# Kernel optimization log

Hardware: AMD Instinct MI355X
Metric: run time of the kernel (lower is better)

Reference implementation:

```python
import jax, jax.numpy as jnp
import numpy as np

B, H, S, D = 4, 16, 2048, 128

def setup_inputs() -> dict:
    key = jax.random.key(0)
    ks = jax.random.split(key, 7)
    inv = 1.0 / np.sqrt(D)
    return {
        "x1": jax.random.normal(ks[0], (B, H, S, D), dtype=jnp.float32),
        "Wq": jax.random.normal(ks[1], (D, D), dtype=jnp.float32) * inv,
        "bq": jax.random.normal(ks[2], (D,), dtype=jnp.float32) * 0.02,
        "Wk": jax.random.normal(ks[3], (D, D), dtype=jnp.float32) * inv,
        "bk": jax.random.normal(ks[4], (D,), dtype=jnp.float32) * 0.02,
        "Wv": jax.random.normal(ks[5], (D, D), dtype=jnp.float32) * inv,
        "bv": jax.random.normal(ks[6], (D,), dtype=jnp.float32) * 0.02,
    }

def reference(x1, Wq, bq, Wk, bk, Wv, bv):
    # torch.nn.Linear: y = x @ W.T + b  (applied to last dim per-head)
    q = jnp.einsum('bhsd,ed->bhse', x1, Wq) + bq
    k = jnp.einsum('bhsd,ed->bhse', x1, Wk) + bk
    v = jnp.einsum('bhsd,ed->bhse', x1, Wv) + bv
    # NOTE: original applies NO 1/sqrt(d) scaling — kept faithful.
    qk = jnp.einsum('bhqd,bhkd->bhqk', q, k)          # [B,H,S,S]
    attn = jax.nn.softmax(qk, axis=-1)
    # dropout(p=0.5) treated as identity (eval mode) for determinism
    out = jnp.einsum('bhqk,bhkd->bhqd', attn, v)      # [B,H,S,D]
    out = jnp.transpose(out, (0, 2, 1, 3)).reshape(B, S * H, D)
    return out
```

## Files before the change

kernel.cpp:

```cpp
#include <hip/hip_runtime.h>
#include <hip/hip_bf16.h>

#define S_LEN 2048
#define D_DIM 128
#define H_NUM 16

typedef float f32x4 __attribute__((ext_vector_type(4)));
typedef _Float16 f16x8 __attribute__((ext_vector_type(8)));
typedef _Float16 f16x4 __attribute__((ext_vector_type(4)));

__device__ __forceinline__ _Float16 f2h(float f) { return (_Float16)f; }

__global__ __launch_bounds__(256) void wconv_kernel(
    const float* __restrict__ Wq, const float* __restrict__ Wk,
    const float* __restrict__ Wv, _Float16* __restrict__ Wb) {
    int i = blockIdx.x * 256 + threadIdx.x;
    Wb[i]         = f2h(Wq[i]);
    Wb[16384 + i] = f2h(Wk[i]);
    Wb[32768 + i] = f2h(Wv[i]);
}

__global__ __launch_bounds__(256) void proj_kernel(
    const float* __restrict__ x,
    const float* __restrict__ bq, const float* __restrict__ bk,
    const float* __restrict__ bv,
    const _Float16* __restrict__ Wb,
    _Float16* __restrict__ Qg, _Float16* __restrict__ Kg, _Float16* __restrict__ Vt)
{
    const int blk = blockIdx.x;
    const int bh  = blk >> 4;
    const int st  = blk & 15;
    const int tid = threadIdx.x;
    const int w = tid >> 6, lane = tid & 63, g = lane >> 4, r16 = lane & 15;
    const int base = st * 128 + w * 32;

    f16x8 xf[2][4];
    #pragma unroll
    for (int rs = 0; rs < 2; ++rs) {
        const int row = base + rs * 16 + r16;
        const float* xr = x + (size_t)(bh * S_LEN + row) * D_DIM + g * 8;
        #pragma unroll
        for (int kk = 0; kk < 4; ++kk) {
            float4 a = *(const float4*)(xr + kk * 32);
            float4 b = *(const float4*)(xr + kk * 32 + 4);
            f16x8 f;
            f[0]=f2h(a.x); f[1]=f2h(a.y); f[2]=f2h(a.z); f[3]=f2h(a.w);
            f[4]=f2h(b.x); f[5]=f2h(b.y); f[6]=f2h(b.z); f[7]=f2h(b.w);
            xf[rs][kk] = f;
        }
    }

    #pragma unroll 1
    for (int p = 0; p < 3; ++p) {
        const float* bias = (p == 0) ? bq : (p == 1) ? bk : bv;
        const _Float16* W = Wb + p * 16384;
        f32x4 acc[2][8];
        #pragma unroll
        for (int rs = 0; rs < 2; ++rs)
            #pragma unroll
            for (int et = 0; et < 8; ++et)
                acc[rs][et] = (f32x4){0.f, 0.f, 0.f, 0.f};

        #pragma unroll
        for (int et = 0; et < 8; ++et) {
            const _Float16* wr = W + (size_t)(et * 16 + r16) * 128 + g * 8;
            #pragma unroll
            for (int kk = 0; kk < 4; ++kk) {
                f16x8 wf = *(const f16x8*)(wr + kk * 32);
                acc[0][et] = __builtin_amdgcn_mfma_f32_16x16x32_f16(xf[0][kk], wf, acc[0][et], 0, 0, 0);
                acc[1][et] = __builtin_amdgcn_mfma_f32_16x16x32_f16(xf[1][kk], wf, acc[1][et], 0, 0, 0);
            }
        }

        #pragma unroll
        for (int et = 0; et < 8; ++et) {
            const float be = bias[et * 16 + r16];
            #pragma unroll
            for (int rs = 0; rs < 2; ++rs) {
                const int row0 = base + rs * 16 + g * 4;
                if (p == 2) {
                    f16x4 vv;
                    vv[0] = f2h(acc[rs][et][0] + be);
                    vv[1] = f2h(acc[rs][et][1] + be);
                    vv[2] = f2h(acc[rs][et][2] + be);
                    vv[3] = f2h(acc[rs][et][3] + be);
                    *(f16x4*)(Vt + (size_t)bh * D_DIM * S_LEN
                                 + (size_t)(et * 16 + r16) * S_LEN + row0) = vv;
                } else {
                    _Float16* O = (p == 0) ? Qg : Kg;
                    #pragma unroll
                    for (int i = 0; i < 4; ++i)
                        O[(size_t)(bh * S_LEN + row0 + i) * D_DIM + et * 16 + r16]
                            = f2h(acc[rs][et][i] + be);
                }
            }
        }
    }
}

__global__ __launch_bounds__(256) void attn_kernel(
    const _Float16* __restrict__ Qg, const _Float16* __restrict__ Kg,
    const _Float16* __restrict__ Vt, float* __restrict__ out)
{
    __shared__ _Float16 k_lds[64][144];
    __shared__ _Float16 v_lds[128][80];
    __shared__ _Float16 p_lds[4][16][80];

    const int blk = blockIdx.x;
    const int bh = blk >> 5;
    const int qt = blk & 31;
    const int b = bh >> 4, h = bh & 15;
    const int tid = threadIdx.x;
    const int w = tid >> 6, lane = tid & 63, g = lane >> 4, r16 = lane & 15;

    f16x8 qf[4];
    {
        const int qrow = qt * 64 + w * 16 + r16;
        const _Float16* qp = Qg + (size_t)(bh * S_LEN + qrow) * D_DIM + g * 8;
        #pragma unroll
        for (int kk = 0; kk < 4; ++kk) qf[kk] = *(const f16x8*)(qp + kk * 32);
    }

    f32x4 acc[8];
    #pragma unroll
    for (int dt = 0; dt < 8; ++dt) acc[dt] = (f32x4){0.f, 0.f, 0.f, 0.f};
    float m[4], l[4];
    #pragma unroll
    for (int i = 0; i < 4; ++i) { m[i] = -1e30f; l[i] = 0.f; }

    const _Float16* Kb = Kg + (size_t)bh * S_LEN * D_DIM;
    const _Float16* Vb = Vt + (size_t)bh * D_DIM * S_LEN;
    const float LOG2E = 1.4426950408889634f;

    for (int kv = 0; kv < 32; ++kv) {
        #pragma unroll
        for (int cc = 0; cc < 4; ++cc) {
            const int off = (tid + cc * 256) * 8;
            const int r = off >> 7, c = off & 127;
            *(uint4*)&k_lds[r][c] =
                *(const uint4*)(Kb + (size_t)(kv * 64 + r) * D_DIM + c);
            const int d = off >> 6, c2 = off & 63;
            *(uint4*)&v_lds[d][c2] =
                *(const uint4*)(Vb + (size_t)d * S_LEN + kv * 64 + c2);
        }
        __syncthreads();

        f32x4 sacc[4];
        #pragma unroll
        for (int ct = 0; ct < 4; ++ct) sacc[ct] = (f32x4){0.f, 0.f, 0.f, 0.f};
        #pragma unroll
        for (int kk = 0; kk < 4; ++kk) {
            f16x8 qk = qf[kk];
            #pragma unroll
            for (int ct = 0; ct < 4; ++ct) {
                f16x8 kf = *(const f16x8*)&k_lds[ct * 16 + r16][kk * 32 + g * 8];
                sacc[ct] = __builtin_amdgcn_mfma_f32_16x16x32_f16(qk, kf, sacc[ct], 0, 0, 0);
            }
        }

        float alpha[4], rsum[4];
        #pragma unroll
        for (int i = 0; i < 4; ++i) {
            float t = fmaxf(fmaxf(sacc[0][i], sacc[1][i]),
                            fmaxf(sacc[2][i], sacc[3][i]));
            t = fmaxf(t, __shfl_xor(t, 1, 64));
            t = fmaxf(t, __shfl_xor(t, 2, 64));
            t = fmaxf(t, __shfl_xor(t, 4, 64));
            t = fmaxf(t, __shfl_xor(t, 8, 64));
            const float nm = fmaxf(m[i], t);
            alpha[i] = exp2f((m[i] - nm) * LOG2E);
            m[i] = nm;
            rsum[i] = 0.f;
        }
        #pragma unroll
        for (int ct = 0; ct < 4; ++ct) {
            #pragma unroll
            for (int i = 0; i < 4; ++i) {
                const float pv = exp2f((sacc[ct][i] - m[i]) * LOG2E);
                rsum[i] += pv;
                p_lds[w][g * 4 + i][ct * 16 + r16] = f2h(pv);
            }
        }
        #pragma unroll
        for (int i = 0; i < 4; ++i) {
            float t = rsum[i];
            t += __shfl_xor(t, 1, 64);
            t += __shfl_xor(t, 2, 64);
            t += __shfl_xor(t, 4, 64);
            t += __shfl_xor(t, 8, 64);
            l[i] = l[i] * alpha[i] + t;
        }
        #pragma unroll
        for (int dt = 0; dt < 8; ++dt)
            #pragma unroll
            for (int i = 0; i < 4; ++i)
                acc[dt][i] *= alpha[i];

        f16x8 pf[2];
        #pragma unroll
        for (int ks = 0; ks < 2; ++ks)
            pf[ks] = *(const f16x8*)&p_lds[w][r16][ks * 32 + g * 8];
        #pragma unroll
        for (int ks = 0; ks < 2; ++ks) {
            #pragma unroll
            for (int dt = 0; dt < 8; ++dt) {
                f16x8 vf = *(const f16x8*)&v_lds[dt * 16 + r16][ks * 32 + g * 8];
                acc[dt] = __builtin_amdgcn_mfma_f32_16x16x32_f16(pf[ks], vf, acc[dt], 0, 0, 0);
            }
        }
        __syncthreads();
    }

    #pragma unroll
    for (int dt = 0; dt < 8; ++dt) {
        #pragma unroll
        for (int i = 0; i < 4; ++i) {
            const int s = qt * 64 + w * 16 + g * 4 + i;
            out[(((size_t)b * S_LEN + s) * H_NUM + h) * D_DIM + dt * 16 + r16]
                = acc[dt][i] / l[i];
        }
    }
}

extern "C" void kernel_launch(void* const* d_in, const int* in_sizes, int n_in,
                              void* d_out, int out_size, void* d_ws, size_t ws_size,
                              hipStream_t stream) {
    const float* x  = (const float*)d_in[0];
    const float* Wq = (const float*)d_in[1];
    const float* bq = (const float*)d_in[2];
    const float* Wk = (const float*)d_in[3];
    const float* bk = (const float*)d_in[4];
    const float* Wv = (const float*)d_in[5];
    const float* bv = (const float*)d_in[6];
    float* out = (float*)d_out;

    char* ws = (char*)d_ws;
    _Float16* Wb  = (_Float16*)ws;
    _Float16* Qg  = (_Float16*)(ws + 131072);
    _Float16* Kg  = Qg + (size_t)64 * S_LEN * D_DIM;
    _Float16* Vtg = Kg + (size_t)64 * S_LEN * D_DIM;

    wconv_kernel<<<64, 256, 0, stream>>>(Wq, Wk, Wv, Wb);
    proj_kernel<<<1024, 256, 0, stream>>>(x, bq, bk, bv, Wb, Qg, Kg, Vtg);
    attn_kernel<<<2048, 256, 0, stream>>>(Qg, Kg, Vtg, out);
}
```

Before: 625.2 us.

## Double query tile per wave, prefetch K/V into registers, transpose score MFMA

The attention kernel now handles 128 query rows per block, 32 per wave, so each K/V tile loaded into LDS is reused twice as much, and the grid is halved. The next K/V tile is prefetched into registers while the current one is computed, overlapping global loads with MFMA work. Scores are computed as K·Q^T so each lane holds a full query column, which makes the softmax reductions cheaper, and P is written with a swizzled vectorized store. The Q/K projection likewise swaps MFMA operands to produce vectorized f16x4 row stores. The cost is higher register pressure from the doubled accumulators and the prefetch registers, which may reduce occupancy.

```diff
diff --git a/kernel.cpp b/kernel.cpp
--- a/kernel.cpp
+++ b/kernel.cpp
@@ -67,31 +67,41 @@
             #pragma unroll
             for (int kk = 0; kk < 4; ++kk) {
                 f16x8 wf = *(const f16x8*)(wr + kk * 32);
-                acc[0][et] = __builtin_amdgcn_mfma_f32_16x16x32_f16(xf[0][kk], wf, acc[0][et], 0, 0, 0);
-                acc[1][et] = __builtin_amdgcn_mfma_f32_16x16x32_f16(xf[1][kk], wf, acc[1][et], 0, 0, 0);
+                if (p < 2) {
+                    acc[0][et] = __builtin_amdgcn_mfma_f32_16x16x32_f16(wf, xf[0][kk], acc[0][et], 0, 0, 0);
+                    acc[1][et] = __builtin_amdgcn_mfma_f32_16x16x32_f16(wf, xf[1][kk], acc[1][et], 0, 0, 0);
+                } else {
+                    acc[0][et] = __builtin_amdgcn_mfma_f32_16x16x32_f16(xf[0][kk], wf, acc[0][et], 0, 0, 0);
+                    acc[1][et] = __builtin_amdgcn_mfma_f32_16x16x32_f16(xf[1][kk], wf, acc[1][et], 0, 0, 0);
+                }
             }
         }
 
         #pragma unroll
         for (int et = 0; et < 8; ++et) {
-            const float be = bias[et * 16 + r16];
             #pragma unroll
             for (int rs = 0; rs < 2; ++rs) {
-                const int row0 = base + rs * 16 + g * 4;
-                if (p == 2) {
+                if (p < 2) {
+                    const int srow = base + rs * 16 + r16;
+                    const int e0 = et * 16 + g * 4;
+                    float4 b4 = *(const float4*)(bias + e0);
+                    f16x4 o;
+                    o[0] = f2h(acc[rs][et][0] + b4.x);
+                    o[1] = f2h(acc[rs][et][1] + b4.y);
+                    o[2] = f2h(acc[rs][et][2] + b4.z);
+                    o[3] = f2h(acc[rs][et][3] + b4.w);
+                    _Float16* O = (p == 0) ? Qg : Kg;
+                    *(f16x4*)(O + (size_t)(bh * S_LEN + srow) * D_DIM + e0) = o;
+                } else {
+                    const float be = bias[et * 16 + r16];
+                    const int s0 = base + rs * 16 + g * 4;
                     f16x4 vv;
                     vv[0] = f2h(acc[rs][et][0] + be);
                     vv[1] = f2h(acc[rs][et][1] + be);
                     vv[2] = f2h(acc[rs][et][2] + be);
                     vv[3] = f2h(acc[rs][et][3] + be);
                     *(f16x4*)(Vt + (size_t)bh * D_DIM * S_LEN
-                                 + (size_t)(et * 16 + r16) * S_LEN + row0) = vv;
-                } else {
-                    _Float16* O = (p == 0) ? Qg : Kg;
-                    #pragma unroll
-                    for (int i = 0; i < 4; ++i)
-                        O[(size_t)(bh * S_LEN + row0 + i) * D_DIM + et * 16 + r16]
-                            = f2h(acc[rs][et][i] + be);
+                                 + (size_t)(et * 16 + r16) * S_LEN + s0) = vv;
                 }
             }
         }
@@ -102,122 +112,145 @@
     const _Float16* __restrict__ Qg, const _Float16* __restrict__ Kg,
     const _Float16* __restrict__ Vt, float* __restrict__ out)
 {
-    __shared__ _Float16 k_lds[64][144];
-    __shared__ _Float16 v_lds[128][80];
-    __shared__ _Float16 p_lds[4][16][80];
+    __shared__ _Float16 k_lds[64][136];
+    __shared__ _Float16 v_lds[128][72];
+    __shared__ _Float16 p_lds[4][32 * 64];
 
     const int blk = blockIdx.x;
-    const int bh = blk >> 5;
-    const int qt = blk & 31;
+    const int bh = blk >> 4;
+    const int qt = blk & 15;
     const int b = bh >> 4, h = bh & 15;
     const int tid = threadIdx.x;
     const int w = tid >> 6, lane = tid & 63, g = lane >> 4, r16 = lane & 15;
-
-    f16x8 qf[4];
-    {
-        const int qrow = qt * 64 + w * 16 + r16;
+    const int swz = (r16 & 7) << 3;
+
+    f16x8 qf[2][4];
+    #pragma unroll
+    for (int s = 0; s < 2; ++s) {
+        const int qrow = qt * 128 + w * 32 + s * 16 + r16;
         const _Float16* qp = Qg + (size_t)(bh * S_LEN + qrow) * D_DIM + g * 8;
         #pragma unroll
-        for (int kk = 0; kk < 4; ++kk) qf[kk] = *(const f16x8*)(qp + kk * 32);
-    }
-
-    f32x4 acc[8];
-    #pragma unroll
-    for (int dt = 0; dt < 8; ++dt) acc[dt] = (f32x4){0.f, 0.f, 0.f, 0.f};
-    float m[4], l[4];
-    #pragma unroll
-    for (int i = 0; i < 4; ++i) { m[i] = -1e30f; l[i] = 0.f; }
-
-    const _Float16* Kb = Kg + (size_t)bh * S_LEN * D_DIM;
+        for (int kk = 0; kk < 4; ++kk) qf[s][kk] = *(const f16x8*)(qp + kk * 32);
+    }
+
+    f32x4 acc[2][8];
+    #pragma unroll
+    for (int s = 0; s < 2; ++s)
+        #pragma unroll
+        for (int dt = 0; dt < 8; ++dt) acc[s][dt] = (f32x4){0.f, 0.f, 0.f, 0.f};
+    float m[2] = {-1e30f, -1e30f}, l[2] = {0.f, 0.f};
+
+    const _Float16* Kb = Qg ? Kg + (size_t)bh * S_LEN * D_DIM : Kg;
     const _Float16* Vb = Vt + (size_t)bh * D_DIM * S_LEN;
     const float LOG2E = 1.4426950408889634f;
 
+    uint4 kreg[4], vreg[4];
+    #pragma unroll
+    for (int cc = 0; cc < 4; ++cc) {
+        const int off = (tid + cc * 256) * 8;
+        kreg[cc] = *(const uint4*)(Kb + (size_t)(off >> 7) * D_DIM + (off & 127));
+        vreg[cc] = *(const uint4*)(Vb + (size_t)(off >> 6) * S_LEN + (off & 63));
+    }
+
     for (int kv = 0; kv < 32; ++kv) {
+        __syncthreads();
         #pragma unroll
         for (int cc = 0; cc < 4; ++cc) {
             const int off = (tid + cc * 256) * 8;
-            const int r = off >> 7, c = off & 127;
-            *(uint4*)&k_lds[r][c] =
-                *(const uint4*)(Kb + (size_t)(kv * 64 + r) * D_DIM + c);
-            const int d = off >> 6, c2 = off & 63;
-            *(uint4*)&v_lds[d][c2] =
-                *(const uint4*)(Vb + (size_t)d * S_LEN + kv * 64 + c2);
+            *(uint4*)&k_lds[off >> 7][off & 127] = kreg[cc];
+            *(uint4*)&v_lds[off >> 6][off & 63] = vreg[cc];
         }
         __syncthreads();
-
-        f32x4 sacc[4];
-        #pragma unroll
-        for (int ct = 0; ct < 4; ++ct) sacc[ct] = (f32x4){0.f, 0.f, 0.f, 0.f};
-        #pragma unroll
-        for (int kk = 0; kk < 4; ++kk) {
-            f16x8 qk = qf[kk];
+        if (kv + 1 < 32) {
+            #pragma unroll
+            for (int cc = 0; cc < 4; ++cc) {
+                const int off = (tid + cc * 256) * 8;
+                kreg[cc] = *(const uint4*)(Kb + (size_t)((kv + 1) * 64 + (off >> 7)) * D_DIM + (off & 127));
+                vreg[cc] = *(const uint4*)(Vb + (size_t)(off >> 6) * S_LEN + (kv + 1) * 64 + (off & 63));
+            }
+        }
+
+        f32x4 sacc[2][4];
+        #pragma unroll
+        for (int s = 0; s < 2; ++s)
+            #pragma unroll
+            for (int ct = 0; ct < 4; ++ct) sacc[s][ct] = (f32x4){0.f, 0.f, 0.f, 0.f};
+        #pragma unroll
+        for (int ct = 0; ct < 4; ++ct) {
+            #pragma unroll
+            for (int kk = 0; kk < 4; ++kk) {
+                f16x8 kf = *(const f16x8*)&k_lds[ct * 16 + r16][kk * 32 + g * 8];
+                sacc[0][ct] = __builtin_amdgcn_mfma_f32_16x16x32_f16(kf, qf[0][kk], sacc[0][ct], 0, 0, 0);
+                sacc[1][ct] = __builtin_amdgcn_mfma_f32_16x16x32_f16(kf, qf[1][kk], sacc[1][ct], 0, 0, 0);
+            }
+        }
+
+        #pragma unroll
+        for (int s = 0; s < 2; ++s) {
+            float t = sacc[s][0][0];
+            #pragma unroll
+            for (int ct = 0; ct < 4; ++ct)
+                #pragma unroll
+                for (int i = 0; i < 4; ++i) t = fmaxf(t, sacc[s][ct][i]);
+            t = fmaxf(t, __shfl_xor(t, 16, 64));
+            t = fmaxf(t, __shfl_xor(t, 32, 64));
+            const float nm = fmaxf(m[s], t);
+            const float al = exp2f((m[s] - nm) * LOG2E);
+            m[s] = nm;
+
+            float rsum = 0.f;
+            _Float16* prow = &p_lds[w][(s * 16 + r16) * 64];
             #pragma unroll
             for (int ct = 0; ct < 4; ++ct) {
-                f16x8 kf = *(const f16x8*)&k_lds[ct * 16 + r16][kk * 32 + g * 8];
-                sacc[ct] = __builtin_amdgcn_mfma_f32_16x16x32_f16(qk, kf, sacc[ct], 0, 0, 0);
-            }
-        }
-
-        float alpha[4], rsum[4];
-        #pragma unroll
-        for (int i = 0; i < 4; ++i) {
-            float t = fmaxf(fmaxf(sacc[0][i], sacc[1][i]),
-                            fmaxf(sacc[2][i], sacc[3][i]));
-            t = fmaxf(t, __shfl_xor(t, 1, 64));
-            t = fmaxf(t, __shfl_xor(t, 2, 64));
-            t = fmaxf(t, __shfl_xor(t, 4, 64));
-            t = fmaxf(t, __shfl_xor(t, 8, 64));
-            const float nm = fmaxf(m[i], t);
-            alpha[i] = exp2f((m[i] - nm) * LOG2E);
-            m[i] = nm;
-            rsum[i] = 0.f;
-        }
-        #pragma unroll
-        for (int ct = 0; ct < 4; ++ct) {
+                f16x4 ph;
+                #pragma unroll
+                for (int i = 0; i < 4; ++i) {
+                    const float pv = exp2f((sacc[s][ct][i] - nm) * LOG2E);
+                    rsum += pv;
+                    ph[i] = f2h(pv);
+                }
+                *(f16x4*)&prow[(ct * 16 + g * 4) ^ swz] = ph;
+            }
+            rsum += __shfl_xor(rsum, 16, 64);
+            rsum += __shfl_xor(rsum, 32, 64);
+            l[s] = l[s] * al + rsum;
+
             #pragma unroll
             for (int i = 0; i < 4; ++i) {
-                const float pv = exp2f((sacc[ct][i] - m[i]) * LOG2E);
-                rsum[i] += pv;
-                p_lds[w][g * 4 + i][ct * 16 + r16] = f2h(pv);
-            }
-        }
-        #pragma unroll
-        for (int i = 0; i < 4; ++i) {
-            float t = rsum[i];
-            t += __shfl_xor(t, 1, 64);
-            t += __shfl_xor(t, 2, 64);
-            t += __shfl_xor(t, 4, 64);
-            t += __shfl_xor(t, 8, 64);
-            l[i] = l[i] * alpha[i] + t;
-        }
-        #pragma unroll
-        for (int dt = 0; dt < 8; ++dt)
-            #pragma unroll
-            for (int i = 0; i < 4; ++i)
-                acc[dt][i] *= alpha[i];
-
-        f16x8 pf[2];
-        #pragma unroll
-        for (int ks = 0; ks < 2; ++ks)
-            pf[ks] = *(const f16x8*)&p_lds[w][r16][ks * 32 + g * 8];
+                const float ab = __shfl(al, g * 4 + i, 64);
+                #pragma unroll
+                for (int dt = 0; dt < 8; ++dt) acc[s][dt][i] *= ab;
+            }
+        }
+
+        f16x8 pf[2][2];
+        #pragma unroll
+        for (int s = 0; s < 2; ++s)
+            #pragma unroll
+            for (int ks = 0; ks < 2; ++ks)
+                pf[s][ks] = *(const f16x8*)&p_lds[w][(s * 16 + r16) * 64 + ((ks * 32 + g * 8) ^ swz)];
         #pragma unroll
         for (int ks = 0; ks < 2; ++ks) {
             #pragma unroll
             for (int dt = 0; dt < 8; ++dt) {
                 f16x8 vf = *(const f16x8*)&v_lds[dt * 16 + r16][ks * 32 + g * 8];
-                acc[dt] = __builtin_amdgcn_mfma_f32_16x16x32_f16(pf[ks], vf, acc[dt], 0, 0, 0);
-            }
-        }
-        __syncthreads();
-    }
-
-    #pragma unroll
-    for (int dt = 0; dt < 8; ++dt) {
+                acc[0][dt] = __builtin_amdgcn_mfma_f32_16x16x32_f16(pf[0][ks], vf, acc[0][dt], 0, 0, 0);
+                acc[1][dt] = __builtin_amdgcn_mfma_f32_16x16x32_f16(pf[1][ks], vf, acc[1][dt], 0, 0, 0);
+            }
+        }
+    }
+
+    #pragma unroll
+    for (int s = 0; s < 2; ++s) {
         #pragma unroll
         for (int i = 0; i < 4; ++i) {
-            const int s = qt * 64 + w * 16 + g * 4 + i;
-            out[(((size_t)b * S_LEN + s) * H_NUM + h) * D_DIM + dt * 16 + r16]
-                = acc[dt][i] / l[i];
+            const float li = __shfl(l[s], g * 4 + i, 64);
+            const float inv = 1.f / li;
+            const int sg = qt * 128 + w * 32 + s * 16 + g * 4 + i;
+            #pragma unroll
+            for (int dt = 0; dt < 8; ++dt)
+                out[(((size_t)b * S_LEN + sg) * H_NUM + h) * D_DIM + dt * 16 + r16]
+                    = acc[s][dt][i] * inv;
         }
     }
 }
@@ -242,5 +275,5 @@
 
     wconv_kernel<<<64, 256, 0, stream>>>(Wq, Wk, Wv, Wb);
     proj_kernel<<<1024, 256, 0, stream>>>(x, bq, bk, bv, Wb, Qg, Kg, Vtg);
-    attn_kernel<<<2048, 256, 0, stream>>>(Qg, Kg, Vtg, out);
-}
+    attn_kernel<<<1024, 256, 0, stream>>>(Qg, Kg, Vtg, out);
+}
```

Measured after the change: 963.0 us. 54.0% more time.
